# Kernel tuning notes

Hardware: AMD Instinct MI355X
Metric: run time of the kernel (lower is better)

Reference implementation:

```python
import jax, jax.numpy as jnp
import numpy as np

VISION_TOKEN_TYPE = 1

def _swiglu_mlp(x, w_gate, w_up, w_down):
    # x: [B, L, D]; w_gate/w_up: [D, F]; w_down: [F, D]
    g = jax.nn.silu(jnp.einsum('bld,df->blf', x, w_gate))
    u = jnp.einsum('bld,df->blf', x, w_up)
    return jnp.einsum('blf,fd->bld', g * u, w_down)

def _vision_mask(token_type_ids):
    # vision_token_mask[:, :-1] = (tt[:, :-1]==V) & (tt[:, 1:]==V); last col False
    is_v = token_type_ids == VISION_TOKEN_TYPE
    pair = is_v[:, :-1] & is_v[:, 1:]
    return jnp.concatenate([pair, jnp.zeros_like(pair[:, :1])], axis=1)  # [B, L] bool

def setup_inputs() -> dict:
    key = jax.random.key(0)
    ks = jax.random.split(key, 8)
    B, L, D, F = 2, 2048, 4096, 11008
    s = 0.02
    return {
        'hidden_states': jax.random.normal(ks[0], (B, L, D), dtype=jnp.float32),
        'token_type_ids': jax.random.randint(ks[1], (B, L), 0, 2, dtype=jnp.int64),
        'vision_gate': jax.random.normal(ks[2], (D, F), dtype=jnp.float32) * s,
        'vision_up': jax.random.normal(ks[3], (D, F), dtype=jnp.float32) * s,
        'vision_down': jax.random.normal(ks[4], (F, D), dtype=jnp.float32) * s,
        'language_gate': jax.random.normal(ks[5], (D, F), dtype=jnp.float32) * s,
        'language_up': jax.random.normal(ks[6], (D, F), dtype=jnp.float32) * s,
        'language_down': jax.random.normal(ks[7], (F, D), dtype=jnp.float32) * s,
    }

def reference(hidden_states, token_type_ids, vision_gate, vision_up, vision_down,
              language_gate, language_up, language_down):
    vmask = _vision_mask(token_type_ids)  # [B, L]
    out_v = _swiglu_mlp(hidden_states, vision_gate, vision_up, vision_down)
    out_l = _swiglu_mlp(hidden_states, language_gate, language_up, language_down)
    return jnp.where(vmask[:, :, None], out_v, out_l)
```

## Files before the change

kernel.cpp:

```cpp
#include <hip/hip_runtime.h>
#include <hip/hip_bf16.h>

#define B_    2
#define L_    2048
#define D_    4096
#define F_    11008
#define M_TOK (B_ * L_)
#define BM    256
#define M_ALLOC (M_TOK + BM)
#define NTM   (M_ALLOC / BM)
#define NT_GU (D_ / 64)
#define NT_DN (F_ / 64)
#define NTILE_F (F_ / 128)
#define SPLITK_DN 4
#define LDS_GU 131072
#define LDS_DN 131072

typedef __attribute__((ext_vector_type(8))) __bf16 bf16x8;
typedef __attribute__((ext_vector_type(4))) float  f32x4;
typedef unsigned short ushort_t;
typedef unsigned int   uint_t;


__device__ __forceinline__ void gload_lds16(const void* g, void* l) {
  __builtin_amdgcn_global_load_lds(
      (const __attribute__((address_space(1))) void*)g,
      (__attribute__((address_space(3))) void*)l, 16, 0, 0);
}

#define PH_BAR()  { __builtin_amdgcn_sched_barrier(0); __builtin_amdgcn_s_barrier(); __builtin_amdgcn_sched_barrier(0); }
#define LGKM0()   { asm volatile("s_waitcnt lgkmcnt(0)" ::: "memory"); __builtin_amdgcn_sched_barrier(0); }
#define LGKM8()   { asm volatile("s_waitcnt lgkmcnt(8)" ::: "memory"); __builtin_amdgcn_sched_barrier(0); }
#define LGKM4()   { asm volatile("s_waitcnt lgkmcnt(4)" ::: "memory"); __builtin_amdgcn_sched_barrier(0); }
#define VM4()     { asm volatile("s_waitcnt vmcnt(4)" ::: "memory"); __builtin_amdgcn_sched_barrier(0); }
#define VM0()     { asm volatile("s_waitcnt vmcnt(0)" ::: "memory"); __builtin_amdgcn_sched_barrier(0); }

__device__ __forceinline__ ushort_t f2bf(float v) {
  union { __hip_bfloat16 h; ushort_t u; } cv;
  cv.h = __float2bfloat16(v);
  return cv.u;
}

__device__ __forceinline__ int xcd_swz(int orig, int nwg) {
  const int q = nwg >> 3, r = nwg & 7, xcd = orig & 7;
  return (xcd < r ? xcd * (q + 1) : r * (q + 1) + (xcd - r) * q) + (orig >> 3);
}

__device__ __forceinline__ void stage_half(const __hip_bfloat16* __restrict__ src, int ldE,
                                           __bf16* ldsb, int w, int lane) {
#pragma unroll
  for (int j = 0; j < 2; ++j) {
    const int ch  = (w * 2 + j) * 64 + lane;
    const int row = ch >> 3;
    const int cc  = (ch & 7) ^ (row & 7);
    gload_lds16(src + (size_t)(row * ldE + cc * 8), ldsb + (w * 2 + j) * 512);
  }
}

__device__ __forceinline__ bf16x8 ldfrag(const __bf16* region, int row, int koffb) {
  const int off = ((row << 7) + koffb) ^ ((row & 7) << 4);
  return *(const bf16x8*)((const char*)region + off);
}

__device__ __forceinline__ void mfma_q(f32x4 (&acc)[8][4], int mb, int nb,
                                       const bf16x8 (&af)[4][2], const bf16x8 (&bf)[2][2]) {
#pragma unroll
  for (int mm = 0; mm < 4; ++mm)
#pragma unroll
    for (int nn = 0; nn < 2; ++nn)
#pragma unroll
      for (int ks = 0; ks < 2; ++ks)
        acc[mb + mm][nb + nn] = __builtin_amdgcn_mfma_f32_16x16x32_bf16(
            af[mm][ks], bf[nn][ks], acc[mb + mm][nb + nn], 0, 0, 0);
}

__device__ __forceinline__ void gemm_kloop(const __hip_bfloat16* __restrict__ Ag, const int ldA,
                                           const __hip_bfloat16* __restrict__ Bg, const int ldB,
                                           const int nt, __bf16* smem, f32x4 (&acc)[8][4],
                                           const int wm, const int wn, const int l15,
                                           const int l4, const int w, const int lane) {
  stage_half(Ag,             ldA, smem,                w, lane);
  stage_half(Ag + 128 * ldA, ldA, smem + 8192,         w, lane);
  stage_half(Bg,             ldB, smem + 16384,        w, lane);
  stage_half(Bg + 128 * ldB, ldB, smem + 24576,        w, lane);
  if (1 < nt) {
    stage_half(Ag + 64,             ldA, smem + 32768,        w, lane);
    stage_half(Ag + 64 + 128 * ldA, ldA, smem + 32768 + 8192, w, lane);
  }
  VM4(); PH_BAR();

  for (int t = 0; t < nt; ++t) {
    __bf16* bufc = smem + (t & 1) * 32768;
    __bf16* bufn = smem + ((t + 1) & 1) * 32768;
    const __bf16* At = bufc;
    const __bf16* Bt = bufc + 16384;
    bf16x8 a0[4][2], a1[4][2], b0[2][2], b1[2][2];

#pragma unroll
    for (int i = 0; i < 4; ++i)
#pragma unroll
      for (int ks = 0; ks < 2; ++ks)
        a0[i][ks] = ldfrag(At, wm * 128 + i * 16 + l15, ks * 64 + l4 * 16);
#pragma unroll
    for (int n = 0; n < 2; ++n)
#pragma unroll
      for (int ks = 0; ks < 2; ++ks)
        b0[n][ks] = ldfrag(Bt, wn * 64 + n * 16 + l15, ks * 64 + l4 * 16);
    if (t + 1 < nt) stage_half(Bg + (t + 1) * 64, ldB, bufn + 16384, w, lane);
    LGKM8(); PH_BAR(); LGKM0();
    __builtin_amdgcn_s_setprio(1);
    mfma_q(acc, 0, 0, a0, b0);
    __builtin_amdgcn_s_setprio(0);
    PH_BAR();

#pragma unroll
    for (int i = 0; i < 4; ++i)
#pragma unroll
      for (int ks = 0; ks < 2; ++ks)
        a1[i][ks] = ldfrag(At, wm * 128 + 64 + i * 16 + l15, ks * 64 + l4 * 16);
    if (t + 1 < nt) stage_half(Bg + (t + 1) * 64 + 128 * ldB, ldB, bufn + 24576, w, lane);
    LGKM4(); PH_BAR(); LGKM0();
    __builtin_amdgcn_s_setprio(1);
    mfma_q(acc, 4, 0, a1, b0);
    __builtin_amdgcn_s_setprio(0);
    PH_BAR();

#pragma unroll
    for (int n = 0; n < 2; ++n)
#pragma unroll
      for (int ks = 0; ks < 2; ++ks)
        b1[n][ks] = ldfrag(Bt, wn * 64 + 32 + n * 16 + l15, ks * 64 + l4 * 16);
    if (t + 2 < nt) stage_half(Ag + (t + 2) * 64, ldA, bufc, w, lane);
    PH_BAR(); LGKM0();
    __builtin_amdgcn_s_setprio(1);
    mfma_q(acc, 4, 2, a1, b1);
    __builtin_amdgcn_s_setprio(0);
    PH_BAR();

    if (t + 2 < nt) stage_half(Ag + (t + 2) * 64 + 128 * ldA, ldA, bufc + 8192, w, lane);
    __builtin_amdgcn_s_setprio(1);
    mfma_q(acc, 0, 2, a0, b1);
    __builtin_amdgcn_s_setprio(0);
    if (t + 2 < nt) { VM4(); } else { VM0(); }
    PH_BAR();
  }
}


__global__ void init_kernel(int* counters, int* slot2tok) {
  int i = blockIdx.x * 256 + threadIdx.x;
  if (i < 2) counters[i] = 0;
  if (i < M_ALLOC) slot2tok[i] = -1;
}

__global__ void assign_kernel(const int* __restrict__ tt, int* counters,
                              int* __restrict__ slot2tok) {
  int t = blockIdx.x * 256 + threadIdx.x;
  if (t >= M_TOK) return;
  int l = t & (L_ - 1);
  bool isv = (tt[t] == 1) && (l < L_ - 1) && (tt[t + 1] == 1);
  int slot;
  if (isv) slot = atomicAdd(&counters[0], 1);
  else     slot = M_ALLOC - 1 - atomicAdd(&counters[1], 1);
  slot2tok[slot] = t;
}

__global__ void gather_cvt(const float* __restrict__ x, const int* __restrict__ slot2tok,
                           __hip_bfloat16* __restrict__ xg) {
  const int s = blockIdx.x;
  const int t = slot2tok[s];
  __hip_bfloat16* dst = xg + (size_t)s * D_ + threadIdx.x * 16;
  union { ushort_t h[8]; uint4 v; } p0, p1;
  if (t >= 0) {
    const float4* s4 = (const float4*)(x + (size_t)t * D_ + threadIdx.x * 16);
    float4 a = s4[0], b = s4[1], c = s4[2], d = s4[3];
    float vals[16] = {a.x,a.y,a.z,a.w,b.x,b.y,b.z,b.w,c.x,c.y,c.z,c.w,d.x,d.y,d.z,d.w};
#pragma unroll
    for (int i = 0; i < 8; ++i) p0.h[i] = f2bf(vals[i]);
#pragma unroll
    for (int i = 0; i < 8; ++i) p1.h[i] = f2bf(vals[8 + i]);
  } else {
    p0.v = make_uint4(0, 0, 0, 0);
    p1.v = make_uint4(0, 0, 0, 0);
  }
  *(uint4*)dst = p0.v;
  *(uint4*)(dst + 8) = p1.v;
}

__global__ __launch_bounds__(128) void transpose_cvt64(const float* __restrict__ in,
                                                       __hip_bfloat16* __restrict__ out,
                                                       int R, int C) {
  const int c  = threadIdx.x & 63;
  const int rc = threadIdx.x >> 6;
  const int c0 = blockIdx.x * 64;
  const int r0 = blockIdx.y * 64 + rc * 32;
  const float* ip = in + (size_t)r0 * C + c0 + c;
  uint_t pk[16];
#pragma unroll
  for (int j = 0; j < 16; ++j) {
    float v0 = ip[(size_t)(2 * j) * C];
    float v1 = ip[(size_t)(2 * j + 1) * C];
    pk[j] = (uint_t)f2bf(v0) | ((uint_t)f2bf(v1) << 16);
  }
  uint4* op = (uint4*)(out + (size_t)(c0 + c) * R + r0);
#pragma unroll
  for (int k = 0; k < 4; ++k)
    op[k] = make_uint4(pk[4 * k], pk[4 * k + 1], pk[4 * k + 2], pk[4 * k + 3]);
}

__global__ void sentinel_kernel(float* out, int n) {
  int i = blockIdx.x * 256 + threadIdx.x;
  if (i < n) out[i] = 1e30f;
}

__global__ __launch_bounds__(512, 2) void gemm256_gateup_fused(
    const __hip_bfloat16* __restrict__ Xg,
    const __hip_bfloat16* __restrict__ WgTv, const __hip_bfloat16* __restrict__ WuTv,
    const __hip_bfloat16* __restrict__ WgTl, const __hip_bfloat16* __restrict__ WuTl,
    __hip_bfloat16* __restrict__ H, const int* __restrict__ counters) {
  extern __shared__ __bf16 smem[];
  const int tid = threadIdx.x, lane = tid & 63, w = tid >> 6;
  const int wm = w >> 1, wn = w & 1;
  const int l15 = lane & 15, l4 = lane >> 4;

  const int wg = xcd_swz(blockIdx.x, gridDim.x);
  const int mt = wg % NTM, ntile = wg / NTM;
  const int row0 = mt * BM;
  const int ncol0 = ntile * 128;
  const int nv = counters[0];
  const bool isv = row0 < nv;
  const __hip_bfloat16* Ag   = Xg + (size_t)row0 * D_;
  const __hip_bfloat16* Bg_g = (isv ? WgTv : WgTl) + (size_t)ncol0 * D_;
  const __hip_bfloat16* Bu_g = (isv ? WuTv : WuTl) + (size_t)ncol0 * D_;

  f32x4 accg[4][4] = {};
  f32x4 accu[4][4] = {};
  const int nt = NT_GU;

  stage_half(Ag,                  D_, smem,          w, lane);
  stage_half(Ag + 128 * D_,       D_, smem + 8192,   w, lane);
  stage_half(Bg_g,                D_, smem + 32768,  w, lane);
  stage_half(Bu_g,                D_, smem + 49152,  w, lane);
  stage_half(Ag + 64,             D_, smem + 16384,  w, lane);
  stage_half(Ag + 64 + 128 * D_,  D_, smem + 24576,  w, lane);
  VM4(); PH_BAR();

  for (int t = 0; t < nt; ++t) {
    const int cur = t & 1;
    const __bf16* At  = smem + cur * 16384;
    const __bf16* Bgt = smem + 32768 + cur * 8192;
    const __bf16* But = smem + 49152 + cur * 8192;
    __bf16* nxA  = smem + cur * 16384;
    __bf16* nxBg = smem + 32768 + (cur ^ 1) * 8192;
    __bf16* nxBu = smem + 49152 + (cur ^ 1) * 8192;
    bf16x8 af[4][2], bb[4][2];

#pragma unroll
    for (int m = 0; m < 2; ++m)
#pragma unroll
      for (int ks = 0; ks < 2; ++ks)
        af[m][ks] = ldfrag(At, wm * 64 + m * 16 + l15, ks * 64 + l4 * 16);
#pragma unroll
    for (int n = 0; n < 4; ++n)
#pragma unroll
      for (int ks = 0; ks < 2; ++ks)
        bb[n][ks] = ldfrag(Bgt, wn * 64 + n * 16 + l15, ks * 64 + l4 * 16);
    if (t + 1 < nt) stage_half(Bg_g + (t + 1) * 64, D_, nxBg, w, lane);
    LGKM8(); PH_BAR(); LGKM0();
    __builtin_amdgcn_s_setprio(1);
#pragma unroll
    for (int m = 0; m < 2; ++m)
#pragma unroll
      for (int n = 0; n < 4; ++n)
#pragma unroll
        for (int ks = 0; ks < 2; ++ks)
          accg[m][n] = __builtin_amdgcn_mfma_f32_16x16x32_bf16(
              af[m][ks], bb[n][ks], accg[m][n], 0, 0, 0);
    __builtin_amdgcn_s_setprio(0);
    PH_BAR();

#pragma unroll
    for (int m = 2; m < 4; ++m)
#pragma unroll
      for (int ks = 0; ks < 2; ++ks)
        af[m][ks] = ldfrag(At, wm * 64 + m * 16 + l15, ks * 64 + l4 * 16);
    if (t + 1 < nt) stage_half(Bu_g + (t + 1) * 64, D_, nxBu, w, lane);
    PH_BAR(); LGKM0();
    __builtin_amdgcn_s_setprio(1);
#pragma unroll
    for (int m = 2; m < 4; ++m)
#pragma unroll
      for (int n = 0; n < 4; ++n)
#pragma unroll
        for (int ks = 0; ks < 2; ++ks)
          accg[m][n] = __builtin_amdgcn_mfma_f32_16x16x32_bf16(
              af[m][ks], bb[n][ks], accg[m][n], 0, 0, 0);
    __builtin_amdgcn_s_setprio(0);
    PH_BAR();

#pragma unroll
    for (int n = 0; n < 4; ++n)
#pragma unroll
      for (int ks = 0; ks < 2; ++ks)
        bb[n][ks] = ldfrag(But, wn * 64 + n * 16 + l15, ks * 64 + l4 * 16);
    if (t + 2 < nt) stage_half(Ag + (t + 2) * 64, D_, nxA, w, lane);
    LGKM4(); PH_BAR(); LGKM0();
    __builtin_amdgcn_s_setprio(1);
#pragma unroll
    for (int m = 0; m < 2; ++m)
#pragma unroll
      for (int n = 0; n < 4; ++n)
#pragma unroll
        for (int ks = 0; ks < 2; ++ks)
          accu[m][n] = __builtin_amdgcn_mfma_f32_16x16x32_bf16(
              af[m][ks], bb[n][ks], accu[m][n], 0, 0, 0);
    __builtin_amdgcn_s_setprio(0);
    PH_BAR();

    if (t + 2 < nt) stage_half(Ag + (t + 2) * 64 + 128 * D_, D_, nxA + 8192, w, lane);
    __builtin_amdgcn_s_setprio(1);
#pragma unroll
    for (int m = 2; m < 4; ++m)
#pragma unroll
      for (int n = 0; n < 4; ++n)
#pragma unroll
        for (int ks = 0; ks < 2; ++ks)
          accu[m][n] = __builtin_amdgcn_mfma_f32_16x16x32_bf16(
              af[m][ks], bb[n][ks], accu[m][n], 0, 0, 0);
    __builtin_amdgcn_s_setprio(0);
    if (t + 2 < nt) { VM4(); } else { VM0(); }
    PH_BAR();
  }

#pragma unroll
  for (int m = 0; m < 4; ++m) {
    const int grow = row0 + wm * 64 + m * 16 + l4 * 4;
#pragma unroll
    for (int rr = 0; rr < 4; ++rr) {
      __hip_bfloat16* orow = H + (size_t)(grow + rr) * F_ + ncol0 + wn * 64 + l15;
#pragma unroll
      for (int n = 0; n < 4; ++n) {
        const float g = accg[m][n][rr];
        const float u = accu[m][n][rr];
        orow[n * 16] = __float2bfloat16(g / (1.0f + __expf(-g)) * u);
      }
    }
  }
}


__global__ __launch_bounds__(512, 2) void gemm256_down(
    const __hip_bfloat16* __restrict__ H,
    const __hip_bfloat16* __restrict__ WdTv, const __hip_bfloat16* __restrict__ WdTl,
    float* __restrict__ out, const int* __restrict__ counters,
    const int* __restrict__ slot2tok) {
  extern __shared__ __bf16 smem[];
  const int tid = threadIdx.x, lane = tid & 63, w = tid >> 6;
  const int wm = w >> 2, wn = w & 3;
  const int l15 = lane & 15, l4 = lane >> 4;

  const int wg = xcd_swz(blockIdx.x, gridDim.x);
  const int mt = wg % NTM, ntt = wg / NTM;
  const int z  = blockIdx.y;
  const int row0 = mt * BM;
  const int ncol0 = ntt * 256;
  const int ntz = NT_DN / SPLITK_DN;
  const int t0 = z * ntz;
  const int nv = counters[0];
  const __hip_bfloat16* Bsrc = (row0 < nv) ? WdTv : WdTl;
  const __hip_bfloat16* Ag = H + (size_t)row0 * F_ + t0 * 64;
  const __hip_bfloat16* Bg = Bsrc + (size_t)ncol0 * F_ + t0 * 64;

  f32x4 acc[8][4] = {};
  gemm_kloop(Ag, F_, Bg, F_, ntz, smem, acc, wm, wn, l15, l4, w, lane);

#pragma unroll
  for (int m = 0; m < 8; ++m) {
    const int slot = row0 + wm * 128 + m * 16 + l4 * 4;
#pragma unroll
    for (int rr = 0; rr < 4; ++rr) {
      const int tok = slot2tok[slot + rr];
      if (tok < 0) continue;
      float* orow = out + (size_t)tok * D_ + ncol0 + wn * 64 + l15;
#pragma unroll
      for (int n = 0; n < 4; ++n)
        atomicAdd(&orow[n * 16], acc[m][n][rr]);
    }
  }
}


extern "C" void kernel_launch(void* const* d_in, const int* in_sizes, int n_in,
                              void* d_out, int out_size, void* d_ws, size_t ws_size,
                              hipStream_t stream) {
  const float* x   = (const float*)d_in[0];
  const int*   tt  = (const int*)d_in[1];
  const float* wgv = (const float*)d_in[2];
  const float* wuv = (const float*)d_in[3];
  const float* wdv = (const float*)d_in[4];
  const float* wgl = (const float*)d_in[5];
  const float* wul = (const float*)d_in[6];
  const float* wdl = (const float*)d_in[7];
  float* out = (float*)d_out;

  size_t off = 0;
  auto nalign = [](size_t v) { return (v + 255) & ~(size_t)255; };
  const size_t o_cnt = off; off += nalign(2 * sizeof(int));
  const size_t o_s2t = off; off += nalign((size_t)M_ALLOC * sizeof(int));
  const size_t o_xg  = off; off += nalign((size_t)M_ALLOC * D_ * 2);
  const size_t o_h   = off; off += nalign((size_t)M_ALLOC * F_ * 2);
  const size_t wbytes = nalign((size_t)D_ * F_ * 2);
  const size_t o_wgv = off; off += wbytes;
  const size_t o_wuv = off; off += wbytes;
  const size_t o_wgl = off; off += wbytes;
  const size_t o_wul = off; off += wbytes;

  if (ws_size < off) {
    sentinel_kernel<<<(out_size + 255) / 256, 256, 0, stream>>>(out, out_size);
    return;
  }

  char* ws = (char*)d_ws;
  int* counters = (int*)(ws + o_cnt);
  int* slot2tok = (int*)(ws + o_s2t);
  __hip_bfloat16* Xg  = (__hip_bfloat16*)(ws + o_xg);
  __hip_bfloat16* H   = (__hip_bfloat16*)(ws + o_h);
  __hip_bfloat16* WgTv = (__hip_bfloat16*)(ws + o_wgv);
  __hip_bfloat16* WuTv = (__hip_bfloat16*)(ws + o_wuv);
  __hip_bfloat16* WgTl = (__hip_bfloat16*)(ws + o_wgl);
  __hip_bfloat16* WuTl = (__hip_bfloat16*)(ws + o_wul);
  __hip_bfloat16* WdTv = WgTv;
  __hip_bfloat16* WdTl = WuTv;

  hipFuncSetAttribute((const void*)gemm256_gateup_fused,
                      hipFuncAttributeMaxDynamicSharedMemorySize, LDS_GU);
  hipFuncSetAttribute((const void*)gemm256_down,
                      hipFuncAttributeMaxDynamicSharedMemorySize, LDS_DN);

  hipMemsetAsync(out, 0, (size_t)out_size * sizeof(float), stream);

  init_kernel<<<(M_ALLOC + 255) / 256, 256, 0, stream>>>(counters, slot2tok);
  assign_kernel<<<(M_TOK + 255) / 256, 256, 0, stream>>>(tt, counters, slot2tok);
  gather_cvt<<<M_ALLOC, 256, 0, stream>>>(x, slot2tok, Xg);

  dim3 tb(128);
  dim3 tg_gu(F_ / 64, D_ / 64);
  transpose_cvt64<<<tg_gu, tb, 0, stream>>>(wgv, WgTv, D_, F_);
  transpose_cvt64<<<tg_gu, tb, 0, stream>>>(wuv, WuTv, D_, F_);
  transpose_cvt64<<<tg_gu, tb, 0, stream>>>(wgl, WgTl, D_, F_);
  transpose_cvt64<<<tg_gu, tb, 0, stream>>>(wul, WuTl, D_, F_);

  gemm256_gateup_fused<<<dim3(NTM * NTILE_F), 512, LDS_GU, stream>>>(
      Xg, WgTv, WuTv, WgTl, WuTl, H, counters);

  dim3 tg_dn(D_ / 64, F_ / 64);
  transpose_cvt64<<<tg_dn, tb, 0, stream>>>(wdv, WdTv, F_, D_);
  transpose_cvt64<<<tg_dn, tb, 0, stream>>>(wdl, WdTl, F_, D_);

  gemm256_down<<<dim3(NTM * (D_ / 256), SPLITK_DN), 512, LDS_DN, stream>>>(
      H, WdTv, WdTl, out, counters, slot2tok);
}
```

Baseline: 1.640 ms.

## Batch weight transposes through LDS tiles and drop partial LDS waitcnts

```diff
diff --git a/kernel.cpp b/kernel.cpp
--- a/kernel.cpp
+++ b/kernel.cpp
@@ -30,8 +30,6 @@
 
 #define PH_BAR()  { __builtin_amdgcn_sched_barrier(0); __builtin_amdgcn_s_barrier(); __builtin_amdgcn_sched_barrier(0); }
 #define LGKM0()   { asm volatile("s_waitcnt lgkmcnt(0)" ::: "memory"); __builtin_amdgcn_sched_barrier(0); }
-#define LGKM8()   { asm volatile("s_waitcnt lgkmcnt(8)" ::: "memory"); __builtin_amdgcn_sched_barrier(0); }
-#define LGKM4()   { asm volatile("s_waitcnt lgkmcnt(4)" ::: "memory"); __builtin_amdgcn_sched_barrier(0); }
 #define VM4()     { asm volatile("s_waitcnt vmcnt(4)" ::: "memory"); __builtin_amdgcn_sched_barrier(0); }
 #define VM0()     { asm volatile("s_waitcnt vmcnt(0)" ::: "memory"); __builtin_amdgcn_sched_barrier(0); }
 
@@ -107,7 +105,7 @@
       for (int ks = 0; ks < 2; ++ks)
         b0[n][ks] = ldfrag(Bt, wn * 64 + n * 16 + l15, ks * 64 + l4 * 16);
     if (t + 1 < nt) stage_half(Bg + (t + 1) * 64, ldB, bufn + 16384, w, lane);
-    LGKM8(); PH_BAR(); LGKM0();
+    PH_BAR(); LGKM0();
     __builtin_amdgcn_s_setprio(1);
     mfma_q(acc, 0, 0, a0, b0);
     __builtin_amdgcn_s_setprio(0);
@@ -119,7 +117,7 @@
       for (int ks = 0; ks < 2; ++ks)
         a1[i][ks] = ldfrag(At, wm * 128 + 64 + i * 16 + l15, ks * 64 + l4 * 16);
     if (t + 1 < nt) stage_half(Bg + (t + 1) * 64 + 128 * ldB, ldB, bufn + 24576, w, lane);
-    LGKM4(); PH_BAR(); LGKM0();
+    PH_BAR(); LGKM0();
     __builtin_amdgcn_s_setprio(1);
     mfma_q(acc, 4, 0, a1, b0);
     __builtin_amdgcn_s_setprio(0);
@@ -187,25 +185,41 @@
   *(uint4*)(dst + 8) = p1.v;
 }
 
-__global__ __launch_bounds__(128) void transpose_cvt64(const float* __restrict__ in,
-                                                       __hip_bfloat16* __restrict__ out,
-                                                       int R, int C) {
-  const int c  = threadIdx.x & 63;
-  const int rc = threadIdx.x >> 6;
-  const int c0 = blockIdx.x * 64;
-  const int r0 = blockIdx.y * 64 + rc * 32;
-  const float* ip = in + (size_t)r0 * C + c0 + c;
-  uint_t pk[16];
+__global__ __launch_bounds__(256) void transpose_cvt_lds(
+    const float* __restrict__ s0, const float* __restrict__ s1,
+    const float* __restrict__ s2, const float* __restrict__ s3,
+    __hip_bfloat16* __restrict__ d0, __hip_bfloat16* __restrict__ d1,
+    __hip_bfloat16* __restrict__ d2, __hip_bfloat16* __restrict__ d3,
+    int R, int C) {
+  const float* in;
+  __hip_bfloat16* out;
+  switch (blockIdx.y) {
+    case 0:  in = s0; out = d0; break;
+    case 1:  in = s1; out = d1; break;
+    case 2:  in = s2; out = d2; break;
+    default: in = s3; out = d3; break;
+  }
+  __shared__ float tile[64][65];
+  const int cb = C >> 6;
+  const int c0 = (blockIdx.x % cb) * 64;
+  const int r0 = (blockIdx.x / cb) * 64;
+  const int tx = threadIdx.x & 63;
+  const int ty = threadIdx.x >> 6;
 #pragma unroll
   for (int j = 0; j < 16; ++j) {
-    float v0 = ip[(size_t)(2 * j) * C];
-    float v1 = ip[(size_t)(2 * j + 1) * C];
-    pk[j] = (uint_t)f2bf(v0) | ((uint_t)f2bf(v1) << 16);
-  }
-  uint4* op = (uint4*)(out + (size_t)(c0 + c) * R + r0);
-#pragma unroll
-  for (int k = 0; k < 4; ++k)
-    op[k] = make_uint4(pk[4 * k], pk[4 * k + 1], pk[4 * k + 2], pk[4 * k + 3]);
+    const int r = ty + 4 * j;
+    tile[r][tx] = in[(size_t)(r0 + r) * C + c0 + tx];
+  }
+  __syncthreads();
+  const int rr2 = (threadIdx.x & 31) * 2;
+  const int cc  = threadIdx.x >> 5;
+#pragma unroll
+  for (int j = 0; j < 8; ++j) {
+    const int c = cc + 8 * j;
+    const uint_t lo = f2bf(tile[rr2][c]);
+    const uint_t hi = f2bf(tile[rr2 + 1][c]);
+    *(uint_t*)(out + (size_t)(c0 + c) * R + r0 + rr2) = lo | (hi << 16);
+  }
 }
 
 __global__ void sentinel_kernel(float* out, int n) {
@@ -266,7 +280,7 @@
       for (int ks = 0; ks < 2; ++ks)
         bb[n][ks] = ldfrag(Bgt, wn * 64 + n * 16 + l15, ks * 64 + l4 * 16);
     if (t + 1 < nt) stage_half(Bg_g + (t + 1) * 64, D_, nxBg, w, lane);
-    LGKM8(); PH_BAR(); LGKM0();
+    PH_BAR(); LGKM0();
     __builtin_amdgcn_s_setprio(1);
 #pragma unroll
     for (int m = 0; m < 2; ++m)
@@ -304,7 +318,7 @@
       for (int ks = 0; ks < 2; ++ks)
         bb[n][ks] = ldfrag(But, wn * 64 + n * 16 + l15, ks * 64 + l4 * 16);
     if (t + 2 < nt) stage_half(Ag + (t + 2) * 64, D_, nxA, w, lane);
-    LGKM4(); PH_BAR(); LGKM0();
+    PH_BAR(); LGKM0();
     __builtin_amdgcn_s_setprio(1);
 #pragma unroll
     for (int m = 0; m < 2; ++m)
@@ -443,19 +457,16 @@
   assign_kernel<<<(M_TOK + 255) / 256, 256, 0, stream>>>(tt, counters, slot2tok);
   gather_cvt<<<M_ALLOC, 256, 0, stream>>>(x, slot2tok, Xg);
 
-  dim3 tb(128);
-  dim3 tg_gu(F_ / 64, D_ / 64);
-  transpose_cvt64<<<tg_gu, tb, 0, stream>>>(wgv, WgTv, D_, F_);
-  transpose_cvt64<<<tg_gu, tb, 0, stream>>>(wuv, WuTv, D_, F_);
-  transpose_cvt64<<<tg_gu, tb, 0, stream>>>(wgl, WgTl, D_, F_);
-  transpose_cvt64<<<tg_gu, tb, 0, stream>>>(wul, WuTl, D_, F_);
+  dim3 tb(256);
+  const int tblocks = (F_ / 64) * (D_ / 64);
+  transpose_cvt_lds<<<dim3(tblocks, 4), tb, 0, stream>>>(
+      wgv, wuv, wgl, wul, WgTv, WuTv, WgTl, WuTl, D_, F_);
 
   gemm256_gateup_fused<<<dim3(NTM * NTILE_F), 512, LDS_GU, stream>>>(
       Xg, WgTv, WuTv, WgTl, WuTl, H, counters);
 
-  dim3 tg_dn(D_ / 64, F_ / 64);
-  transpose_cvt64<<<tg_dn, tb, 0, stream>>>(wdv, WdTv, F_, D_);
-  transpose_cvt64<<<tg_dn, tb, 0, stream>>>(wdl, WdTl, F_, D_);
+  transpose_cvt_lds<<<dim3(tblocks, 2), tb, 0, stream>>>(
+      wdv, wdl, wdv, wdl, WdTv, WdTl, WdTv, WdTl, F_, D_);
 
   gemm256_down<<<dim3(NTM * (D_ / 256), SPLITK_DN), 512, LDS_DN, stream>>>(
       H, WdTv, WdTl, out, counters, slot2tok);
```

Result: faster. 1.494 ms (-8.9%).
